# Kernel tuning notes

Measured on AMD Instinct MI355X. Metric: run time of the kernel, lower is better.

Reference implementation:

```python
import jax, jax.numpy as jnp
import numpy as np
from jax.scipy.special import logsumexp

B, T, M = 64, 1024, 128  # batch, seq_len, tag_set_size


def setup_inputs() -> dict:
    key = jax.random.key(0)
    kP, kA, kY, kL = jax.random.split(key, 4)
    P = jax.random.normal(kP, (B, T, M), dtype=jnp.float32)
    A = jax.random.normal(kA, (M + 1, M), dtype=jnp.float32)  # rows 0..M-1: transitions, row M: start
    Y = jax.random.randint(kY, (B, T, 1), 0, M).astype(jnp.int32)
    L = jax.random.randint(kL, (B,), 1, T + 1).astype(jnp.int32)  # lengths in [1, T]
    return {"P": P, "A": A, "Y": Y, "L": L}


def _crf_losses(P, A, Y, L):
    b, t, m = P.shape
    y = Y[:, :, 0]                      # [B,T] int labels
    A_trans, A_start = A[:-1], A[-1]    # [M,M], [M]
    b_idx = jnp.arange(b)

    # step 0
    S0 = P[:, 0] + A_start              # [B,M] forward scores
    sY0 = P[b_idx, 0, y[:, 0]] + A_start[y[:, 0]]  # gold path score at t=0
    loss0 = logsumexp(S0, axis=1) - sY0

    Pt = jnp.swapaxes(P, 0, 1)          # [T,B,M] time-major for scan
    yt = jnp.swapaxes(y, 0, 1)          # [T,B]

    def step(carry, xs):
        S_prev, sY_prev = carry
        P_k, y_prev, y_k = xs           # [B,M], [B], [B]
        # S_k[b,j] = logsumexp_i( S_prev[b,i] + A_trans[i,j] + P_k[b,j] )
        S_k = logsumexp(S_prev[:, :, None] + A_trans[None, :, :] + P_k[:, None, :], axis=1)
        sY = sY_prev + P_k[b_idx, y_k] + A_trans[y_prev, y_k]
        loss = logsumexp(S_k, axis=1) - sY
        return (S_k, sY), loss

    (_, _), losses = jax.lax.scan(step, (S0, sY0), (Pt[1:], yt[:-1], yt[1:]))
    all_losses = jnp.concatenate([loss0[None], losses], axis=0)  # [T,B]
    # pick loss at the true sequence end (L-1) for each batch element
    return all_losses[L - 1, b_idx]


def reference(P, A, Y, L):
    return _crf_losses(P, A, Y, L)
```

## Files before the change

kernel.cpp:

```cpp
#include <hip/hip_runtime.h>

#define T_LEN 1024
#define M_DIM 128
#define B_NUM 64

typedef _Float16 h2 __attribute__((ext_vector_type(2)));

#if __has_builtin(__builtin_amdgcn_fdot2)
#define DOT2(a, b, c) __builtin_amdgcn_fdot2((a), (b), (c), false)
#else
__device__ __forceinline__ float DOT2(h2 a, h2 b, float c) {
  return fmaf((float)a.x, (float)b.x, fmaf((float)a.y, (float)b.y, c));
}
#endif

template<int CTRL>
__device__ __forceinline__ float dppmov(float x) {
  int y = __builtin_amdgcn_update_dpp(0, __float_as_int(x), CTRL, 0xf, 0xf, true);
  return __int_as_float(y);
}

__global__ __launch_bounds__(256, 1) void crf_fwd(
    const float* __restrict__ P, const float* __restrict__ A,
    const int* __restrict__ Y, const int* __restrict__ L,
    float* __restrict__ out)
{
  const int b    = blockIdx.x;
  const int tid  = threadIdx.x;
  const int lane = tid & 63;
  const int wid  = tid >> 6;
  const int jl   = lane & 31;
  const int half = lane >> 5;
  const int j    = wid * 32 + jl;

  __shared__ __align__(16) h2    u_lds[2][80];
  __shared__ __align__(16) float red[2][4];
  __shared__ __align__(16) float red_sum[4];
  __shared__ __align__(16) float sY_sh[4];
  __shared__ __align__(16) float boot[4];

  const int Lb = L[b];
  const float* Pb = P + (size_t)b * T_LEN * M_DIM;
  const int*   Yb = Y + b * T_LEN;

#define BARRIER_RELAXED() do { \
    asm volatile("s_waitcnt lgkmcnt(0)" ::: "memory"); \
    __builtin_amdgcn_s_barrier(); } while (0)

  h2 wpk[32];
  #pragma unroll
  for (int k = 0; k < 8; ++k) {
    #pragma unroll
    for (int e = 0; e < 4; ++e) {
      const int i = (half * 32 + k * 4 + e) * 2;
      h2 hv;
      hv.x = (_Float16)__expf(A[i * M_DIM + j]);
      hv.y = (_Float16)__expf(A[(i + 1) * M_DIM + j]);
      wpk[k * 4 + e] = hv;
    }
  }

  const int wslot_m = wid * 16 + (jl >> 1);
  const int wslot   = wslot_m < 32 ? wslot_m : 36 + (wslot_m - 32);
  const bool writer = (half == 0) && !(jl & 1);

  float mySY = 0.f;
  for (int tt = tid; tt < Lb; tt += 256) {
    int yt = Yb[tt];
    float term = Pb[tt * M_DIM + yt];
    term += (tt == 0) ? A[M_DIM * M_DIM + yt] : A[Yb[tt - 1] * M_DIM + yt];
    mySY += term;
  }
  #pragma unroll
  for (int d = 1; d < 64; d <<= 1) mySY += __shfl_xor(mySY, d);
  if (lane == 0) sY_sh[wid] = mySY;

  float s0 = Pb[j] + A[M_DIM * M_DIM + j];
  {
    float mm = s0;
    #pragma unroll
    for (int d = 1; d <= 16; d <<= 1) mm = fmaxf(mm, __shfl_xor(mm, d));
    if (lane == 0) boot[wid] = mm;
  }
  if (tid < 4) red[1][tid] = 1.0f;
  __syncthreads();
  float C = fmaxf(fmaxf(boot[0], boot[1]), fmaxf(boot[2], boot[3]));
  float un = __expf(s0 - C);
  {
    float nb = __shfl_xor(un, 1);
    if (writer) {
      h2 hv; hv.x = (_Float16)un; hv.y = (_Float16)nb;
      u_lds[0][wslot] = hv;
    }
  }
  float p_cur = Pb[M_DIM + j];
  if (Lb == 1) {
    float zs = un;
    #pragma unroll
    for (int d = 1; d <= 16; d <<= 1) zs += __shfl_xor(zs, d);
    if (lane == 0) red_sum[wid] = zs;
  }
  __syncthreads();
  if (Lb == 1) goto finish;

#define CRF_STEP(S, PAR, PNEXT)                                            \
  {                                                                        \
    const float4* u4 = (const float4*)(u_lds[cur]);                        \
    float4 rz = *(const float4*)(&red[PAR][0]);                            \
    float Z  = fmaxf(fmaxf(rz.x, rz.y), fmaxf(rz.z, rz.w));                \
    float ep = __expf(p_cur) * __builtin_amdgcn_rcpf(Z) * 0.00390625f;     \
    C += __logf(Z) + 5.54517744f;                      \
    float acc0 = 0.f, acc1 = 0.f, acc2 = 0.f, acc3 = 0.f;                  \
    _Pragma("unroll")                                                      \
    for (int k = 0; k < 8; ++k) {                                          \
      float4 uu = u4[half * 9 + k];                                        \
      acc0 = DOT2(__builtin_bit_cast(h2, uu.x), wpk[k * 4 + 0], acc0);     \
      acc1 = DOT2(__builtin_bit_cast(h2, uu.y), wpk[k * 4 + 1], acc1);     \
      acc2 = DOT2(__builtin_bit_cast(h2, uu.z), wpk[k * 4 + 2], acc2);     \
      acc3 = DOT2(__builtin_bit_cast(h2, uu.w), wpk[k * 4 + 3], acc3);     \
    }                                                                      \
    float v = (acc0 + acc1) + (acc2 + acc3);                               \
    v += __shfl_xor(v, 32);                                                \
    un = v * ep;                                                           \
    {                                                                      \
      float nb = __shfl_xor(un, 1);                                        \
      if (writer) {                                                        \
        h2 hv; hv.x = (_Float16)un; hv.y = (_Float16)nb;                   \
        u_lds[cur ^ 1][wslot] = hv;                                        \
      }                                                                    \
    }                                                                      \
    {                     \
      float zm = un;                                                       \
      zm = fmaxf(zm, dppmov<0xB1>(zm));                          \
      zm = fmaxf(zm, dppmov<0x4E>(zm));                          \
      zm = fmaxf(zm, dppmov<0x141>(zm));          \
      zm = fmaxf(zm, dppmov<0x140>(zm));               \
      zm = fmaxf(zm, dppmov<0x142>(zm));     \
      if (lane == 16) red[(PAR) ^ 1][wid] = zm;                            \
    }                                                                      \
    const bool last_ = (tb + (S) == Lb - 1);                               \
    if (last_) {                                                           \
      float zs = un;                                                       \
      _Pragma("unroll")                                                    \
      for (int d = 1; d <= 16; d <<= 1) zs += __shfl_xor(zs, d);           \
      if (lane == 0) red_sum[wid] = zs;                                    \
    }                                                                      \
    BARRIER_RELAXED();                                                     \
    if (last_) goto finish;                                                \
    p_cur = (PNEXT);                                                       \
    cur ^= 1;                                                              \
  }

  {
    int cur = 0;
    int tb  = 1;
    for (;;) {
      float pn0, pn1, pn2, pn3, pn4, pn5, pn6, pn7;
      {
        const float* Pq = Pb + j;
        int r;
        r = tb + 1; r = r < T_LEN ? r : T_LEN - 1; pn0 = Pq[r * M_DIM];
        r = tb + 2; r = r < T_LEN ? r : T_LEN - 1; pn1 = Pq[r * M_DIM];
        r = tb + 3; r = r < T_LEN ? r : T_LEN - 1; pn2 = Pq[r * M_DIM];
        r = tb + 4; r = r < T_LEN ? r : T_LEN - 1; pn3 = Pq[r * M_DIM];
        r = tb + 5; r = r < T_LEN ? r : T_LEN - 1; pn4 = Pq[r * M_DIM];
        r = tb + 6; r = r < T_LEN ? r : T_LEN - 1; pn5 = Pq[r * M_DIM];
        r = tb + 7; r = r < T_LEN ? r : T_LEN - 1; pn6 = Pq[r * M_DIM];
        r = tb + 8; r = r < T_LEN ? r : T_LEN - 1; pn7 = Pq[r * M_DIM];
      }
      CRF_STEP(0, 1, pn0)
      CRF_STEP(1, 0, pn1)
      CRF_STEP(2, 1, pn2)
      CRF_STEP(3, 0, pn3)
      CRF_STEP(4, 1, pn4)
      CRF_STEP(5, 0, pn5)
      CRF_STEP(6, 1, pn6)
      CRF_STEP(7, 0, pn7)
      tb += 8;
    }
  }

finish:
  if (tid == 0) {
    float s  = (red_sum[0] + red_sum[1]) + (red_sum[2] + red_sum[3]);
    float sy = (sY_sh[0] + sY_sh[1]) + (sY_sh[2] + sY_sh[3]);
    out[b] = __logf(s) + C - sy;
  }
}

extern "C" void kernel_launch(void* const* d_in, const int* in_sizes, int n_in,
                              void* d_out, int out_size, void* d_ws, size_t ws_size,
                              hipStream_t stream) {
  const float* P = (const float*)d_in[0];
  const float* A = (const float*)d_in[1];
  const int*   Y = (const int*)d_in[2];
  const int*   L = (const int*)d_in[3];
  float* o = (float*)d_out;
  hipLaunchKernelGGL(crf_fwd, dim3(B_NUM), dim3(256), 0, stream, P, A, Y, L, o);
}
```

Before: 474.7 us.

## Split each tag's dot product across four lanes with 512-thread blocks

Doubles the block to 512 threads so each output tag j is handled by four adjacent lanes, each covering 32 of the 128 source tags (16 packed fp16 pairs), where before two half-waves each covered 64. The partial sums are combined with DPP row shuffles instead of a cross-half shfl_xor, and the packed fp16 state vector and max reduction now use DPP neighbour moves. This halves the serial per-step dot-product length and register weight footprint to shorten the latency-bound recurrence. In exchange the per-step barrier now synchronises 8 waves instead of 4, which may add barrier cost.

```diff
diff --git a/kernel.cpp b/kernel.cpp
--- a/kernel.cpp
+++ b/kernel.cpp
@@ -15,12 +15,17 @@
 #endif
 
 template<int CTRL>
-__device__ __forceinline__ float dppmov(float x) {
+__device__ __forceinline__ float dpp_mov(float x) {
   int y = __builtin_amdgcn_update_dpp(0, __float_as_int(x), CTRL, 0xf, 0xf, true);
   return __int_as_float(y);
 }
 
-__global__ __launch_bounds__(256, 1) void crf_fwd(
+__device__ __forceinline__ unsigned pack_f16(float a, float bq) {
+  h2 hv; hv.x = (_Float16)a; hv.y = (_Float16)bq;
+  return __builtin_bit_cast(unsigned, hv);
+}
+
+__global__ __launch_bounds__(512, 1) void crf_fwd(
     const float* __restrict__ P, const float* __restrict__ A,
     const int* __restrict__ Y, const int* __restrict__ L,
     float* __restrict__ out)
@@ -29,15 +34,14 @@
   const int tid  = threadIdx.x;
   const int lane = tid & 63;
   const int wid  = tid >> 6;
-  const int jl   = lane & 31;
-  const int half = lane >> 5;
-  const int j    = wid * 32 + jl;
-
-  __shared__ __align__(16) h2    u_lds[2][80];
-  __shared__ __align__(16) float red[2][4];
-  __shared__ __align__(16) float red_sum[4];
-  __shared__ __align__(16) float sY_sh[4];
-  __shared__ __align__(16) float boot[4];
+  const int j    = tid >> 2;
+  const int igrp = tid & 3;
+
+  __shared__ __align__(16) unsigned u_pk[2][64];
+  __shared__ __align__(16) float redf[2][16];
+  __shared__ float red_sum[8];
+  __shared__ float sY_sh[8];
+  __shared__ float boot[8];
 
   const int Lb = L[b];
   const float* Pb = P + (size_t)b * T_LEN * M_DIM;
@@ -47,25 +51,18 @@
     asm volatile("s_waitcnt lgkmcnt(0)" ::: "memory"); \
     __builtin_amdgcn_s_barrier(); } while (0)
 
-  h2 wpk[32];
+  h2 w[16];
   #pragma unroll
-  for (int k = 0; k < 8; ++k) {
-    #pragma unroll
-    for (int e = 0; e < 4; ++e) {
-      const int i = (half * 32 + k * 4 + e) * 2;
-      h2 hv;
-      hv.x = (_Float16)__expf(A[i * M_DIM + j]);
-      hv.y = (_Float16)__expf(A[(i + 1) * M_DIM + j]);
-      wpk[k * 4 + e] = hv;
-    }
-  }
-
-  const int wslot_m = wid * 16 + (jl >> 1);
-  const int wslot   = wslot_m < 32 ? wslot_m : 36 + (wslot_m - 32);
-  const bool writer = (half == 0) && !(jl & 1);
+  for (int m = 0; m < 16; ++m) {
+    const int pr = igrp * 16 + m;
+    h2 hv;
+    hv.x = (_Float16)__expf(A[(2 * pr) * M_DIM + j]);
+    hv.y = (_Float16)__expf(A[(2 * pr + 1) * M_DIM + j]);
+    w[m] = hv;
+  }
 
   float mySY = 0.f;
-  for (int tt = tid; tt < Lb; tt += 256) {
+  for (int tt = tid; tt < Lb; tt += 512) {
     int yt = Yb[tt];
     float term = Pb[tt * M_DIM + yt];
     term += (tt == 0) ? A[M_DIM * M_DIM + yt] : A[Yb[tt - 1] * M_DIM + yt];
@@ -79,111 +76,123 @@
   {
     float mm = s0;
     #pragma unroll
-    for (int d = 1; d <= 16; d <<= 1) mm = fmaxf(mm, __shfl_xor(mm, d));
+    for (int d = 1; d < 64; d <<= 1) mm = fmaxf(mm, __shfl_xor(mm, d));
     if (lane == 0) boot[wid] = mm;
   }
-  if (tid < 4) red[1][tid] = 1.0f;
+  if (tid < 16) redf[1][tid] = 1.0f;
   __syncthreads();
-  float C = fmaxf(fmaxf(boot[0], boot[1]), fmaxf(boot[2], boot[3]));
+  float C = boot[0];
+  #pragma unroll
+  for (int q = 1; q < 8; ++q) C = fmaxf(C, boot[q]);
   float un = __expf(s0 - C);
   {
-    float nb = __shfl_xor(un, 1);
-    if (writer) {
-      h2 hv; hv.x = (_Float16)un; hv.y = (_Float16)nb;
-      u_lds[0][wslot] = hv;
-    }
+    float nb = dpp_mov<0x141>(un);
+    if ((tid & 7) == 0) u_pk[0][tid >> 3] = pack_f16(un, nb);
   }
   float p_cur = Pb[M_DIM + j];
   if (Lb == 1) {
-    float zs = un;
+    float s = (igrp == 0) ? un : 0.f;
     #pragma unroll
-    for (int d = 1; d <= 16; d <<= 1) zs += __shfl_xor(zs, d);
-    if (lane == 0) red_sum[wid] = zs;
+    for (int d = 1; d < 64; d <<= 1) s += __shfl_xor(s, d);
+    if (lane == 0) red_sum[wid] = s;
   }
   __syncthreads();
   if (Lb == 1) goto finish;
 
-#define CRF_STEP(S, PAR, PNEXT)                                            \
+#define CRF_STEP(S, PAR, PN)                                               \
   {                                                                        \
-    const float4* u4 = (const float4*)(u_lds[cur]);                        \
-    float4 rz = *(const float4*)(&red[PAR][0]);                            \
-    float Z  = fmaxf(fmaxf(rz.x, rz.y), fmaxf(rz.z, rz.w));                \
-    float ep = __expf(p_cur) * __builtin_amdgcn_rcpf(Z) * 0.00390625f;     \
+    const float4* rf = (const float4*)&redf[PAR][0];                       \
+    float4 ra = rf[0], rb = rf[1], rc = rf[2], rd = rf[3];                 \
+    float Z = fmaxf(fmaxf(fmaxf(ra.x, ra.y), fmaxf(ra.z, ra.w)),           \
+                    fmaxf(fmaxf(rb.x, rb.y), fmaxf(rb.z, rb.w)));          \
+    Z = fmaxf(Z, fmaxf(fmaxf(fmaxf(rc.x, rc.y), fmaxf(rc.z, rc.w)),        \
+                       fmaxf(fmaxf(rd.x, rd.y), fmaxf(rd.z, rd.w))));      \
+    Z = fmaxf(Z, 1e-30f);                                                  \
+    float iZ = __builtin_amdgcn_rcpf(Z) * 0.00390625f;                     \
     C += __logf(Z) + 5.54517744f;                      \
-    float acc0 = 0.f, acc1 = 0.f, acc2 = 0.f, acc3 = 0.f;                  \
-    _Pragma("unroll")                                                      \
-    for (int k = 0; k < 8; ++k) {                                          \
-      float4 uu = u4[half * 9 + k];                                        \
-      acc0 = DOT2(__builtin_bit_cast(h2, uu.x), wpk[k * 4 + 0], acc0);     \
-      acc1 = DOT2(__builtin_bit_cast(h2, uu.y), wpk[k * 4 + 1], acc1);     \
-      acc2 = DOT2(__builtin_bit_cast(h2, uu.z), wpk[k * 4 + 2], acc2);     \
-      acc3 = DOT2(__builtin_bit_cast(h2, uu.w), wpk[k * 4 + 3], acc3);     \
-    }                                                                      \
-    float v = (acc0 + acc1) + (acc2 + acc3);                               \
-    v += __shfl_xor(v, 32);                                                \
+    float ep = __expf(p_cur) * iZ;                                         \
+    const uint4* u4 = (const uint4*)&u_pk[cur][igrp * 16];                 \
+    uint4 uu0 = u4[0], uu1 = u4[1], uu2 = u4[2], uu3 = u4[3];              \
+    float a0 = 0.f, a1 = 0.f, a2 = 0.f, a3 = 0.f;                          \
+    a0 = DOT2(__builtin_bit_cast(h2, uu0.x), w[0],  a0);                   \
+    a1 = DOT2(__builtin_bit_cast(h2, uu0.y), w[1],  a1);                   \
+    a2 = DOT2(__builtin_bit_cast(h2, uu0.z), w[2],  a2);                   \
+    a3 = DOT2(__builtin_bit_cast(h2, uu0.w), w[3],  a3);                   \
+    a0 = DOT2(__builtin_bit_cast(h2, uu1.x), w[4],  a0);                   \
+    a1 = DOT2(__builtin_bit_cast(h2, uu1.y), w[5],  a1);                   \
+    a2 = DOT2(__builtin_bit_cast(h2, uu1.z), w[6],  a2);                   \
+    a3 = DOT2(__builtin_bit_cast(h2, uu1.w), w[7],  a3);                   \
+    a0 = DOT2(__builtin_bit_cast(h2, uu2.x), w[8],  a0);                   \
+    a1 = DOT2(__builtin_bit_cast(h2, uu2.y), w[9],  a1);                   \
+    a2 = DOT2(__builtin_bit_cast(h2, uu2.z), w[10], a2);                   \
+    a3 = DOT2(__builtin_bit_cast(h2, uu2.w), w[11], a3);                   \
+    a0 = DOT2(__builtin_bit_cast(h2, uu3.x), w[12], a0);                   \
+    a1 = DOT2(__builtin_bit_cast(h2, uu3.y), w[13], a1);                   \
+    a2 = DOT2(__builtin_bit_cast(h2, uu3.z), w[14], a2);                   \
+    a3 = DOT2(__builtin_bit_cast(h2, uu3.w), w[15], a3);                   \
+    float v = (a0 + a1) + (a2 + a3);                                       \
+    v += dpp_mov<0xB1>(v);                                  \
+    v += dpp_mov<0x4E>(v);            \
     un = v * ep;                                                           \
     {                                                                      \
-      float nb = __shfl_xor(un, 1);                                        \
-      if (writer) {                                                        \
-        h2 hv; hv.x = (_Float16)un; hv.y = (_Float16)nb;                   \
-        u_lds[cur ^ 1][wslot] = hv;                                        \
-      }                                                                    \
+      float nb = dpp_mov<0x141>(un);     \
+      if ((tid & 7) == 0) u_pk[cur ^ 1][tid >> 3] = pack_f16(un, nb);      \
     }                                                                      \
-    {                     \
+    {                              \
       float zm = un;                                                       \
-      zm = fmaxf(zm, dppmov<0xB1>(zm));                          \
-      zm = fmaxf(zm, dppmov<0x4E>(zm));                          \
-      zm = fmaxf(zm, dppmov<0x141>(zm));          \
-      zm = fmaxf(zm, dppmov<0x140>(zm));               \
-      zm = fmaxf(zm, dppmov<0x142>(zm));     \
-      if (lane == 16) red[(PAR) ^ 1][wid] = zm;                            \
+      zm = fmaxf(zm, dpp_mov<0x141>(zm));                   \
+      zm = fmaxf(zm, dpp_mov<0x140>(zm));                  \
+      zm = fmaxf(zm, dpp_mov<0x142>(zm));          \
+      if (lane == 16) redf[(PAR) ^ 1][2 * wid] = zm;                       \
+      if (lane == 48) redf[(PAR) ^ 1][2 * wid + 1] = zm;                   \
     }                                                                      \
     const bool last_ = (tb + (S) == Lb - 1);                               \
     if (last_) {                                                           \
-      float zs = un;                                                       \
+      float s = (igrp == 0) ? un : 0.f;                                    \
       _Pragma("unroll")                                                    \
-      for (int d = 1; d <= 16; d <<= 1) zs += __shfl_xor(zs, d);           \
-      if (lane == 0) red_sum[wid] = zs;                                    \
+      for (int d = 1; d < 64; d <<= 1) s += __shfl_xor(s, d);              \
+      if (lane == 0) red_sum[wid] = s;                                     \
     }                                                                      \
     BARRIER_RELAXED();                                                     \
     if (last_) goto finish;                                                \
-    p_cur = (PNEXT);                                                       \
+    p_cur = (PN);                                                          \
     cur ^= 1;                                                              \
   }
 
   {
     int cur = 0;
     int tb  = 1;
+    const float* Pq = Pb + j;
     for (;;) {
-      float pn0, pn1, pn2, pn3, pn4, pn5, pn6, pn7;
+      float q0, q1, q2, q3, q4, q5, q6, q7;
       {
-        const float* Pq = Pb + j;
         int r;
-        r = tb + 1; r = r < T_LEN ? r : T_LEN - 1; pn0 = Pq[r * M_DIM];
-        r = tb + 2; r = r < T_LEN ? r : T_LEN - 1; pn1 = Pq[r * M_DIM];
-        r = tb + 3; r = r < T_LEN ? r : T_LEN - 1; pn2 = Pq[r * M_DIM];
-        r = tb + 4; r = r < T_LEN ? r : T_LEN - 1; pn3 = Pq[r * M_DIM];
-        r = tb + 5; r = r < T_LEN ? r : T_LEN - 1; pn4 = Pq[r * M_DIM];
-        r = tb + 6; r = r < T_LEN ? r : T_LEN - 1; pn5 = Pq[r * M_DIM];
-        r = tb + 7; r = r < T_LEN ? r : T_LEN - 1; pn6 = Pq[r * M_DIM];
-        r = tb + 8; r = r < T_LEN ? r : T_LEN - 1; pn7 = Pq[r * M_DIM];
+        r = tb + 1; r = r < T_LEN ? r : T_LEN - 1; q0 = Pq[r * M_DIM];
+        r = tb + 2; r = r < T_LEN ? r : T_LEN - 1; q1 = Pq[r * M_DIM];
+        r = tb + 3; r = r < T_LEN ? r : T_LEN - 1; q2 = Pq[r * M_DIM];
+        r = tb + 4; r = r < T_LEN ? r : T_LEN - 1; q3 = Pq[r * M_DIM];
+        r = tb + 5; r = r < T_LEN ? r : T_LEN - 1; q4 = Pq[r * M_DIM];
+        r = tb + 6; r = r < T_LEN ? r : T_LEN - 1; q5 = Pq[r * M_DIM];
+        r = tb + 7; r = r < T_LEN ? r : T_LEN - 1; q6 = Pq[r * M_DIM];
+        r = tb + 8; r = r < T_LEN ? r : T_LEN - 1; q7 = Pq[r * M_DIM];
       }
-      CRF_STEP(0, 1, pn0)
-      CRF_STEP(1, 0, pn1)
-      CRF_STEP(2, 1, pn2)
-      CRF_STEP(3, 0, pn3)
-      CRF_STEP(4, 1, pn4)
-      CRF_STEP(5, 0, pn5)
-      CRF_STEP(6, 1, pn6)
-      CRF_STEP(7, 0, pn7)
+      CRF_STEP(0, 1, q0)
+      CRF_STEP(1, 0, q1)
+      CRF_STEP(2, 1, q2)
+      CRF_STEP(3, 0, q3)
+      CRF_STEP(4, 1, q4)
+      CRF_STEP(5, 0, q5)
+      CRF_STEP(6, 1, q6)
+      CRF_STEP(7, 0, q7)
       tb += 8;
     }
   }
 
 finish:
   if (tid == 0) {
-    float s  = (red_sum[0] + red_sum[1]) + (red_sum[2] + red_sum[3]);
-    float sy = (sY_sh[0] + sY_sh[1]) + (sY_sh[2] + sY_sh[3]);
+    float s = 0.f, sy = 0.f;
+    #pragma unroll
+    for (int q2 = 0; q2 < 8; ++q2) { s += red_sum[q2]; sy += sY_sh[q2]; }
     out[b] = __logf(s) + C - sy;
   }
 }
@@ -196,5 +205,5 @@
   const int*   Y = (const int*)d_in[2];
   const int*   L = (const int*)d_in[3];
   float* o = (float*)d_out;
-  hipLaunchKernelGGL(crf_fwd, dim3(B_NUM), dim3(256), 0, stream, P, A, Y, L, o);
-}
+  hipLaunchKernelGGL(crf_fwd, dim3(B_NUM), dim3(512), 0, stream, P, A, Y, L, o);
+}
```

Result: slower. 506.1 us (+6.6%).
